# Performance work log

Measured on AMD Instinct MI355X. Metric: run time of the kernel, lower is better.

The kernel has to match this reference:

```python
import jax, jax.numpy as jnp
import numpy as np

B, N, D = 8, 4096, 1024
DEPTH, HEADS, DH = 4, 16, 64
INNER = HEADS * DH          # 1024
NL, NMP = 64, 4             # latents, mean-pooled latents
FF = 4 * D                  # ff_mult=4
EPS = 1e-5


def _ln(x, w, b):
    # nn.LayerNorm over last dim (eps added to biased variance)
    m = x.mean(-1, keepdims=True)
    v = ((x - m) ** 2).mean(-1, keepdims=True)
    return (x - m) * jax.lax.rsqrt(v + EPS) * w + b


def _ln_g(x, g):
    # custom LayerNorm: gamma only, no bias
    m = x.mean(-1, keepdims=True)
    v = ((x - m) ** 2).mean(-1, keepdims=True)
    return (x - m) * jax.lax.rsqrt(v + EPS) * g


def setup_inputs() -> dict:
    key = jax.random.key(0)
    ks = jax.random.split(key, 16)
    g = lambda i, shape: jax.random.normal(ks[i], shape, jnp.float32) * 0.02
    return dict(
        x=jax.random.normal(ks[0], (B, N, D), jnp.float32),
        pos_emb=g(1, (N, D)),                      # rows [0:N] of the embedding table
        latents=jax.random.normal(ks[2], (NL, D), jnp.float32),
        mp_ln_g=jnp.ones((D,), jnp.float32),
        mp_w=g(3, (D, D * NMP)),
        mp_b=jnp.zeros((D * NMP,), jnp.float32),
        ln_x_w=jnp.ones((DEPTH, D), jnp.float32),
        ln_x_b=jnp.zeros((DEPTH, D), jnp.float32),
        ln_lat_w=jnp.ones((DEPTH, D), jnp.float32),
        ln_lat_b=jnp.zeros((DEPTH, D), jnp.float32),
        wq=g(4, (DEPTH, D, INNER)),
        wkv=g(5, (DEPTH, D, 2 * INNER)),
        wo=g(6, (DEPTH, INNER, D)),
        out_ln_w=jnp.ones((DEPTH, D), jnp.float32),
        out_ln_b=jnp.zeros((DEPTH, D), jnp.float32),
        ff_ln1_g=jnp.ones((DEPTH, D), jnp.float32),
        ff_w1=g(7, (DEPTH, D, FF)),
        ff_ln2_g=jnp.ones((DEPTH, FF), jnp.float32),
        ff_w2=g(8, (DEPTH, FF, D)),
    )


def reference(x, pos_emb, latents, mp_ln_g, mp_w, mp_b,
              ln_x_w, ln_x_b, ln_lat_w, ln_lat_b, wq, wkv, wo,
              out_ln_w, out_ln_b, ff_ln1_g, ff_w1, ff_ln2_g, ff_w2):
    b = x.shape[0]
    xp = x + pos_emb                                  # (b, n, d)
    lat = jnp.broadcast_to(latents, (b,) + latents.shape)
    # mean-pooled latents (mask is all-ones -> plain mean over tokens)
    mp = x.mean(axis=1)                               # (b, d)
    mp_lat = (_ln_g(mp, mp_ln_g) @ mp_w + mp_b).reshape(b, NMP, D)
    lat = jnp.concatenate([mp_lat, lat], axis=1)      # (b, NMP+NL, d)
    scale = DH ** -0.5
    for l in range(DEPTH):
        # --- PerceiverAttention ---
        xn = _ln(xp, ln_x_w[l], ln_x_b[l])
        ln_lat = _ln(lat, ln_lat_w[l], ln_lat_b[l])
        q = (ln_lat @ wq[l]).reshape(b, -1, HEADS, DH) * scale   # (b, i, h, dh)
        kv = jnp.concatenate([xn, ln_lat], axis=1) @ wkv[l]      # (b, n+i, 2*inner)
        k, v = jnp.split(kv, 2, axis=-1)
        k = k.reshape(b, -1, HEADS, DH)
        v = v.reshape(b, -1, HEADS, DH)
        sim = jnp.einsum('bihd,bjhd->bhij', q, k)                # (b, h, i, n+i)
        attn = jax.nn.softmax(sim, axis=-1)
        o = jnp.einsum('bhij,bjhd->bihd', attn, v).reshape(b, -1, INNER)
        o = _ln(o @ wo[l], out_ln_w[l], out_ln_b[l])
        lat = lat + o
        # --- feedforward block ---
        h = jax.nn.gelu(_ln_g(lat, ff_ln1_g[l]) @ ff_w1[l], approximate=False)
        lat = lat + _ln_g(h, ff_ln2_g[l]) @ ff_w2[l]
    return lat
```

## Files before the change

kernel.cpp:

```cpp
#include <hip/hip_runtime.h>

typedef __bf16 bf16x8 __attribute__((ext_vector_type(8)));
typedef float f32x4 __attribute__((ext_vector_type(4)));
typedef unsigned short u16;
typedef unsigned int u32;

typedef __attribute__((address_space(3))) u16 lds_u16;
typedef __attribute__((address_space(1))) const u16 glb_u16;

#define NJC 4

__device__ inline float bf2f(u16 u) { union { u32 i; float f; } x; x.i = (u32)u << 16; return x.f; }
__device__ inline u16 f2bf(float f) {
  union { float f; u32 i; } u; u.f = f;
  u32 r = u.i + 0x7fffu + ((u.i >> 16) & 1u);
  return (u16)(r >> 16);
}

__device__ inline float blk_sum256(float v, float* red) {
#pragma unroll
  for (int o = 32; o > 0; o >>= 1) v += __shfl_xor(v, o);
  __syncthreads();
  if ((threadIdx.x & 63) == 0) red[threadIdx.x >> 6] = v;
  __syncthreads();
  return red[0] + red[1] + red[2] + red[3];
}

__global__ __launch_bounds__(512, 1) void gemm_kv(const u16* __restrict__ A,
                                                  const u16* __restrict__ BT,
                                                  u16* __restrict__ C,
                                                  const float* __restrict__ bias) {
  extern __shared__ __align__(16) u16 lds[];
  const int tid = threadIdx.x, l = tid & 63, w = tid >> 6;
  const int wr = w >> 2, wc = w & 3;
  int bid = blockIdx.x;
  int swz = (bid & 7) * 128 + (bid >> 3);
  int by = swz >> 3, bx = swz & 7;
  const long m0 = (long)by * 256;
  const int n0 = bx * 256;

  long srcA[2], srcB[2];
#pragma unroll
  for (int s = 0; s < 2; s++) {
    int g = s * 512 + tid;
    int p = g >> 3, j = g & 7, jp = j ^ (p & 7);
    int row = (p << 1) | (jp >> 2), cc = jp & 3;
    srcA[s] = (m0 + row) * 1024 + cc * 8;
    srcB[s] = ((long)(n0 + row)) * 1024 + cc * 8;
  }
  const int ldsoff[2] = { (w * 64) * 8, (512 + w * 64) * 8 };

  const int rA = l & 15, cch = l >> 4;
  const int R0a = wr * 128 + rA;
  const int aoff = (R0a >> 1) * 64 + (((((R0a & 1) << 2) | cch) ^ ((R0a >> 1) & 7)) << 3);
  const int R0b = wc * 64 + rA;
  const int boff = (R0b >> 1) * 64 + (((((R0b & 1) << 2) | cch) ^ ((R0b >> 1) & 7)) << 3);

  f32x4 acc[8][4] = {};

  auto stage = [&](int t, int ab) {
    u16* dst = lds + (((t & 3) * 2 + ab) << 13);
    const u16* src = ab == 0 ? A : BT;
    const long* so = ab == 0 ? srcA : srcB;
    int kt = t * 32;
#pragma unroll
    for (int s = 0; s < 2; s++)
      __builtin_amdgcn_global_load_lds((glb_u16*)(src + so[s] + kt),
                                       (lds_u16*)(dst + ldsoff[s]), 16, 0, 0);
  };

  stage(0, 0); stage(0, 1); stage(1, 0); stage(1, 1); stage(2, 0); stage(2, 1);
  asm volatile("s_waitcnt vmcnt(8)" ::: "memory");
  __builtin_amdgcn_s_barrier();

  for (int t = 0; t < 16; ++t) {
    const int s = 2 * t;
    const u16* Ab0 = lds + (((s & 3) * 2 + 0) << 13);
    const u16* Bb0 = lds + (((s & 3) * 2 + 1) << 13);
    const u16* Ab1 = lds + ((((s + 1) & 3) * 2 + 0) << 13);
    const u16* Bb1 = lds + ((((s + 1) & 3) * 2 + 1) << 13);
    bf16x8 af[8], b0, b1;

#pragma unroll
    for (int mf = 0; mf < 8; mf++) af[mf] = *(const bf16x8*)(Ab0 + aoff + mf * 512);
    b0 = *(const bf16x8*)(Bb0 + boff);
    b1 = *(const bf16x8*)(Bb0 + boff + 512);
    if (s + 3 < 32) stage(s + 3, 0);
    __builtin_amdgcn_s_barrier();
    asm volatile("s_waitcnt lgkmcnt(0)" ::: "memory");
    __builtin_amdgcn_sched_barrier(0);
    __builtin_amdgcn_s_setprio(1);
#pragma unroll
    for (int mf = 0; mf < 8; mf++) {
      acc[mf][0] = __builtin_amdgcn_mfma_f32_16x16x32_bf16(af[mf], b0, acc[mf][0], 0, 0, 0);
      acc[mf][1] = __builtin_amdgcn_mfma_f32_16x16x32_bf16(af[mf], b1, acc[mf][1], 0, 0, 0);
    }
    __builtin_amdgcn_s_setprio(0);
    __builtin_amdgcn_s_barrier();

    b0 = *(const bf16x8*)(Bb0 + boff + 1024);
    b1 = *(const bf16x8*)(Bb0 + boff + 1536);
    if (s + 3 < 32) stage(s + 3, 1);
    __builtin_amdgcn_s_barrier();
    asm volatile("s_waitcnt lgkmcnt(0)" ::: "memory");
    __builtin_amdgcn_sched_barrier(0);
    __builtin_amdgcn_s_setprio(1);
#pragma unroll
    for (int mf = 0; mf < 8; mf++) {
      acc[mf][2] = __builtin_amdgcn_mfma_f32_16x16x32_bf16(af[mf], b0, acc[mf][2], 0, 0, 0);
      acc[mf][3] = __builtin_amdgcn_mfma_f32_16x16x32_bf16(af[mf], b1, acc[mf][3], 0, 0, 0);
    }
    __builtin_amdgcn_s_setprio(0);
    if (t < 15) asm volatile("s_waitcnt vmcnt(8)" ::: "memory");
    else        asm volatile("s_waitcnt vmcnt(0)" ::: "memory");
    __builtin_amdgcn_s_barrier();

#pragma unroll
    for (int mf = 0; mf < 8; mf++) af[mf] = *(const bf16x8*)(Ab1 + aoff + mf * 512);
    b0 = *(const bf16x8*)(Bb1 + boff);
    b1 = *(const bf16x8*)(Bb1 + boff + 512);
    if (s + 4 < 32) stage(s + 4, 0);
    __builtin_amdgcn_s_barrier();
    asm volatile("s_waitcnt lgkmcnt(0)" ::: "memory");
    __builtin_amdgcn_sched_barrier(0);
    __builtin_amdgcn_s_setprio(1);
#pragma unroll
    for (int mf = 0; mf < 8; mf++) {
      acc[mf][0] = __builtin_amdgcn_mfma_f32_16x16x32_bf16(af[mf], b0, acc[mf][0], 0, 0, 0);
      acc[mf][1] = __builtin_amdgcn_mfma_f32_16x16x32_bf16(af[mf], b1, acc[mf][1], 0, 0, 0);
    }
    __builtin_amdgcn_s_setprio(0);
    __builtin_amdgcn_s_barrier();

    b0 = *(const bf16x8*)(Bb1 + boff + 1024);
    b1 = *(const bf16x8*)(Bb1 + boff + 1536);
    if (s + 4 < 32) stage(s + 4, 1);
    __builtin_amdgcn_s_barrier();
    asm volatile("s_waitcnt lgkmcnt(0)" ::: "memory");
    __builtin_amdgcn_sched_barrier(0);
    __builtin_amdgcn_s_setprio(1);
#pragma unroll
    for (int mf = 0; mf < 8; mf++) {
      acc[mf][2] = __builtin_amdgcn_mfma_f32_16x16x32_bf16(af[mf], b0, acc[mf][2], 0, 0, 0);
      acc[mf][3] = __builtin_amdgcn_mfma_f32_16x16x32_bf16(af[mf], b1, acc[mf][3], 0, 0, 0);
    }
    __builtin_amdgcn_s_setprio(0);
    if (t < 14)       asm volatile("s_waitcnt vmcnt(8)" ::: "memory");
    else if (t == 14) asm volatile("s_waitcnt vmcnt(4)" ::: "memory");
    __builtin_amdgcn_s_barrier();
  }

  const long batch_off = (m0 >> 12) * ((long)4164 * 2048);
  const int rb0 = (int)(m0 & 4095) + wr * 128 + ((l >> 4) << 2);
#pragma unroll
  for (int mf = 0; mf < 8; mf++) {
#pragma unroll
    for (int nf = 0; nf < 4; nf++) {
      int col = n0 + wc * 64 + nf * 16 + (l & 15);
      float bv = bias[col];
#pragma unroll
      for (int rr = 0; rr < 4; rr++) {
        int rloc = rb0 + mf * 16 + rr;
        C[batch_off + (long)rloc * 2048 + col] = f2bf(acc[mf][nf][rr] + bv);
      }
    }
  }
}

template <int MODE, bool BIAS>
__global__ __launch_bounds__(256) void gemm_nt(const u16* __restrict__ A,
                                               const u16* __restrict__ BT,
                                               void* __restrict__ C,
                                               const float* __restrict__ bias,
                                               int M, int N, int K, float alpha,
                                               int RB, long BS, int LDC, int KC) {
  __shared__ __align__(16) u16 As[128 * 64];
  __shared__ __align__(16) u16 Bs[128 * 64];
  int m0 = blockIdx.y * 128, n0 = blockIdx.x * 128;
  int tid = threadIdx.x;
  int l = tid & 63, w = tid >> 6;
  int wr = w >> 1, wc = w & 1;
  f32x4 acc[4][4] = {};

  const int srow = l >> 3;
  const int scol = (l & 7) * 8;
  const int Mc = M - 1;
  const int k0 = blockIdx.z * KC;
  const int k1 = (k0 + KC < K) ? k0 + KC : K;

  for (int kt = k0; kt < k1; kt += 64) {
#pragma unroll
    for (int r = 0; r < 4; r++) {
      int rowg = (r * 4 + w) * 8;
      int arow = m0 + rowg + srow; if (arow > Mc) arow = Mc;
      int brow = n0 + rowg + srow;
      const u16* ag = A + (long)arow * K + kt + scol;
      const u16* bg = BT + (long)brow * K + kt + scol;
      __builtin_amdgcn_global_load_lds((glb_u16*)ag, (lds_u16*)(As + rowg * 64), 16, 0, 0);
      __builtin_amdgcn_global_load_lds((glb_u16*)bg, (lds_u16*)(Bs + rowg * 64), 16, 0, 0);
    }
    __syncthreads();
#pragma unroll
    for (int kk = 0; kk < 2; kk++) {
      bf16x8 af[4], bfv[4];
#pragma unroll
      for (int mf = 0; mf < 4; mf++)
        af[mf] = *(const bf16x8*)(As + (wr * 64 + mf * 16 + (l & 15)) * 64 + kk * 32 + (l >> 4) * 8);
#pragma unroll
      for (int nf = 0; nf < 4; nf++)
        bfv[nf] = *(const bf16x8*)(Bs + (wc * 64 + nf * 16 + (l & 15)) * 64 + kk * 32 + (l >> 4) * 8);
#pragma unroll
      for (int mf = 0; mf < 4; mf++)
#pragma unroll
        for (int nf = 0; nf < 4; nf++)
          acc[mf][nf] = __builtin_amdgcn_mfma_f32_16x16x32_bf16(af[mf], bfv[nf], acc[mf][nf], 0, 0, 0);
    }
    __syncthreads();
  }

#pragma unroll
  for (int mf = 0; mf < 4; mf++) {
#pragma unroll
    for (int nf = 0; nf < 4; nf++) {
      int col = n0 + wc * 64 + nf * 16 + (l & 15);
      float bv = 0.f;
      if (BIAS) bv = bias[col];
#pragma unroll
      for (int rr = 0; rr < 4; rr++) {
        int row = m0 + wr * 64 + mf * 16 + (l >> 4) * 4 + rr;
        if (row < M) {
          float v = acc[mf][nf][rr] * alpha + bv;
          long off = (long)(row / RB) * BS + (long)(row % RB) * LDC + col;
          if (MODE == 0) ((float*)C)[off] = v;
          else if (MODE == 1) ((u16*)C)[off] = f2bf(v);
          else if (MODE == 2) ((float*)C)[off] += v;
          else atomicAdd(&((float*)C)[off], v);
        }
      }
    }
  }
}

__global__ __launch_bounds__(256) void gemm_two(const u16* __restrict__ A,
                                                const u16* __restrict__ BTq,
                                                const u16* __restrict__ BTkv,
                                                u16* __restrict__ Cq,
                                                u16* __restrict__ Ckv) {
  __shared__ __align__(16) u16 As[128 * 64];
  __shared__ __align__(16) u16 Bs[128 * 64];
  const int K = 1024, M = 544;
  int bxr = blockIdx.x;
  const u16* BT; u16* C; float alpha; int RB; long BS; int LDC; int n0;
  if (bxr < 8) { BT = BTq;  C = Cq;  alpha = 0.125f; RB = 544; BS = 0;                 LDC = 1024; n0 = bxr * 128; }
  else         { BT = BTkv; C = Ckv; alpha = 1.f;    RB = 68;  BS = (long)4164 * 2048; LDC = 2048; n0 = (bxr - 8) * 128; }
  int m0 = blockIdx.y * 128;
  int tid = threadIdx.x;
  int l = tid & 63, w = tid >> 6;
  int wr = w >> 1, wc = w & 1;
  f32x4 acc[4][4] = {};

  const int srow = l >> 3;
  const int scol = (l & 7) * 8;
  const int Mc = M - 1;

  for (int kt = 0; kt < K; kt += 64) {
#pragma unroll
    for (int r = 0; r < 4; r++) {
      int rowg = (r * 4 + w) * 8;
      int arow = m0 + rowg + srow; if (arow > Mc) arow = Mc;
      int brow = n0 + rowg + srow;
      const u16* ag = A + (long)arow * K + kt + scol;
      const u16* bg = BT + (long)brow * K + kt + scol;
      __builtin_amdgcn_global_load_lds((glb_u16*)ag, (lds_u16*)(As + rowg * 64), 16, 0, 0);
      __builtin_amdgcn_global_load_lds((glb_u16*)bg, (lds_u16*)(Bs + rowg * 64), 16, 0, 0);
    }
    __syncthreads();
#pragma unroll
    for (int kk = 0; kk < 2; kk++) {
      bf16x8 af[4], bfv[4];
#pragma unroll
      for (int mf = 0; mf < 4; mf++)
        af[mf] = *(const bf16x8*)(As + (wr * 64 + mf * 16 + (l & 15)) * 64 + kk * 32 + (l >> 4) * 8);
#pragma unroll
      for (int nf = 0; nf < 4; nf++)
        bfv[nf] = *(const bf16x8*)(Bs + (wc * 64 + nf * 16 + (l & 15)) * 64 + kk * 32 + (l >> 4) * 8);
#pragma unroll
      for (int mf = 0; mf < 4; mf++)
#pragma unroll
        for (int nf = 0; nf < 4; nf++)
          acc[mf][nf] = __builtin_amdgcn_mfma_f32_16x16x32_bf16(af[mf], bfv[nf], acc[mf][nf], 0, 0, 0);
    }
    __syncthreads();
  }

#pragma unroll
  for (int mf = 0; mf < 4; mf++) {
#pragma unroll
    for (int nf = 0; nf < 4; nf++) {
      int col = n0 + wc * 64 + nf * 16 + (l & 15);
#pragma unroll
      for (int rr = 0; rr < 4; rr++) {
        int row = m0 + wr * 64 + mf * 16 + (l >> 4) * 4 + rr;
        if (row < M) {
          float v = acc[mf][nf][rr] * alpha;
          long off = (long)(row / RB) * BS + (long)(row % RB) * LDC + col;
          C[off] = f2bf(v);
        }
      }
    }
  }
}

__global__ __launch_bounds__(256) void k_transpose(const float* __restrict__ W,
                                                   const float* __restrict__ scale,
                                                   u16* __restrict__ WT, int K, int N,
                                                   long wls, long sls, long tls) {
  __shared__ float tile[32][33];
  int z = blockIdx.z;
  W += (long)z * wls; WT += (long)z * tls;
  if (scale) scale += (long)z * sls;
  int n0 = blockIdx.x * 32, k0 = blockIdx.y * 32;
  int x = threadIdx.x, y = threadIdx.y;
#pragma unroll
  for (int i = 0; i < 4; i++) tile[y + 8 * i][x] = W[(long)(k0 + y + 8 * i) * N + n0 + x];
  __syncthreads();
#pragma unroll
  for (int i = 0; i < 4; i++) {
    int k = k0 + x, n = n0 + y + 8 * i;
    float v = tile[x][y + 8 * i];
    if (scale) v *= scale[k];
    WT[(long)n * K + k] = f2bf(v);
  }
}

__global__ __launch_bounds__(256) void k_transpose2(const float* __restrict__ W,
                                                    const float* __restrict__ scale,
                                                    u16* __restrict__ WTs,
                                                    u16* __restrict__ WTp, int K, int N,
                                                    long wls, long sls, long tls) {
  __shared__ float tile[32][33];
  int z = blockIdx.z;
  W += (long)z * wls; scale += (long)z * sls;
  WTs += (long)z * tls; WTp += (long)z * tls;
  int n0 = blockIdx.x * 32, k0 = blockIdx.y * 32;
  int x = threadIdx.x, y = threadIdx.y;
#pragma unroll
  for (int i = 0; i < 4; i++) tile[y + 8 * i][x] = W[(long)(k0 + y + 8 * i) * N + n0 + x];
  __syncthreads();
#pragma unroll
  for (int i = 0; i < 4; i++) {
    int k = k0 + x, n = n0 + y + 8 * i;
    float v = tile[x][y + 8 * i];
    WTp[(long)n * K + k] = f2bf(v);
    WTs[(long)n * K + k] = f2bf(v * scale[k]);
  }
}

__global__ __launch_bounds__(256) void k_xphat(const float* __restrict__ x,
                                               const float* __restrict__ pos,
                                               u16* __restrict__ xph) {
  __shared__ float red[4];
  long row = blockIdx.x;
  int n = blockIdx.x & 4095;
  const float* xr = x + row * 1024;
  const float* pr = pos + (long)n * 1024;
  float v[4]; float s = 0.f;
#pragma unroll
  for (int i = 0; i < 4; i++) { int c = threadIdx.x + i * 256; v[i] = xr[c] + pr[c]; s += v[i]; }
  float mean = blk_sum256(s, red) * (1.f / 1024.f);
  float s2 = 0.f;
#pragma unroll
  for (int i = 0; i < 4; i++) { float d = v[i] - mean; s2 += d * d; }
  float rs = rsqrtf(blk_sum256(s2, red) * (1.f / 1024.f) + 1e-5f);
#pragma unroll
  for (int i = 0; i < 4; i++) xph[row * 1024 + threadIdx.x + i * 256] = f2bf((v[i] - mean) * rs);
}

__global__ __launch_bounds__(256) void k_mp(const float* __restrict__ x, float* __restrict__ macc) {
  int d = blockIdx.x * 256 + threadIdx.x;
  int nc = blockIdx.y, b = blockIdx.z;
  const float* xb = x + (long)b * 4096 * 1024;
  float s = 0.f;
  for (int n = nc * 256; n < nc * 256 + 256; n++) s += xb[(long)n * 1024 + d];
  atomicAdd(&macc[b * 1024 + d], s);
}

__global__ __launch_bounds__(256) void k_mphat(const float* __restrict__ macc,
                                               const float* __restrict__ g,
                                               float* __restrict__ mphat) {
  __shared__ float red[4];
  int b = blockIdx.x;
  float v[4]; float s = 0.f;
#pragma unroll
  for (int i = 0; i < 4; i++) { v[i] = macc[b * 1024 + threadIdx.x + i * 256] * (1.f / 4096.f); s += v[i]; }
  float mean = blk_sum256(s, red) * (1.f / 1024.f);
  float s2 = 0.f;
#pragma unroll
  for (int i = 0; i < 4; i++) { float d = v[i] - mean; s2 += d * d; }
  float rs = rsqrtf(blk_sum256(s2, red) * (1.f / 1024.f) + 1e-5f);
#pragma unroll
  for (int i = 0; i < 4; i++) {
    int c = threadIdx.x + i * 256;
    mphat[b * 1024 + c] = (v[i] - mean) * rs * g[c];
  }
}

__global__ __launch_bounds__(256) void k_mplat(const float* __restrict__ mphat,
                                               const float* __restrict__ w,
                                               const float* __restrict__ bias,
                                               float* __restrict__ lat) {
  int j = blockIdx.x * 256 + threadIdx.x;
  int b = blockIdx.y;
  const float* mh = mphat + b * 1024;
  float s = bias[j];
  for (int k = 0; k < 1024; k++) s += mh[k] * w[(long)k * 4096 + j];
  lat[(long)b * 69632 + (j >> 10) * 1024 + (j & 1023)] = s;
}

__global__ __launch_bounds__(256) void k_latfill(const float* __restrict__ latents,
                                                 float* __restrict__ lat) {
  int idx = blockIdx.x * 256 + threadIdx.x;
  int b = idx >> 16, rest = idx & 65535;
  lat[(long)b * 69632 + 4096 + rest] = latents[rest];
}

__global__ __launch_bounds__(256) void k_lnrow(const float* __restrict__ in,
                                               const float* __restrict__ w,
                                               const float* __restrict__ bb,
                                               u16* __restrict__ out) {
  __shared__ float red[4];
  long row = blockIdx.x;
  const float* xr = in + row * 1024;
  float v[4]; float s = 0.f;
#pragma unroll
  for (int i = 0; i < 4; i++) { v[i] = xr[threadIdx.x + i * 256]; s += v[i]; }
  float mean = blk_sum256(s, red) * (1.f / 1024.f);
  float s2 = 0.f;
#pragma unroll
  for (int i = 0; i < 4; i++) { float d = v[i] - mean; s2 += d * d; }
  float rs = rsqrtf(blk_sum256(s2, red) * (1.f / 1024.f) + 1e-5f);
#pragma unroll
  for (int i = 0; i < 4; i++) {
    int c = threadIdx.x + i * 256;
    out[row * 1024 + c] = f2bf((v[i] - mean) * rs * w[c] + bb[c]);
  }
}

__global__ __launch_bounds__(256) void k_bias1(const float* __restrict__ wkv,
                                               const float* __restrict__ lnxb,
                                               float* __restrict__ bxp,
                                               long wls, long bls, long pls) {
  int z = blockIdx.z;
  wkv += (long)z * wls; lnxb += (long)z * bls; bxp += (long)z * pls;
  int n = blockIdx.x * 256 + threadIdx.x;
  int kc = blockIdx.y;
  float s = 0.f;
  for (int k = kc * 64; k < kc * 64 + 64; k++) s += lnxb[k] * wkv[(long)k * 2048 + n];
  bxp[kc * 2048 + n] = s;
}
__global__ __launch_bounds__(256) void k_bias2(const float* __restrict__ bxp,
                                               float* __restrict__ bx,
                                               long pls, long xls) {
  int z = blockIdx.y;
  bxp += (long)z * pls; bx += (long)z * xls;
  int n = blockIdx.x * 256 + threadIdx.x;
  float s = 0.f;
#pragma unroll
  for (int kc = 0; kc < 16; kc++) s += bxp[kc * 2048 + n];
  bx[n] = s;
}

__global__ __launch_bounds__(256) void k_flash(const u16* __restrict__ q,
                                               const u16* __restrict__ kv,
                                               float* __restrict__ opart,
                                               float* __restrict__ lpart) {
  int c = blockIdx.x, h = blockIdx.y, b = blockIdx.z;
  int tid = threadIdx.x, l = tid & 63, w = tid >> 6;

  __shared__ __align__(16) char smem_raw[46080];
  u16 (*Vt)[64][40] = reinterpret_cast<u16(*)[64][40]>(smem_raw);
  u16 (*Pl)[80][40] = reinterpret_cast<u16(*)[80][40]>(smem_raw + 20480);
  float (*O_s)[64] = reinterpret_cast<float(*)[64]>(smem_raw);
  float* l_s = reinterpret_cast<float*>(smem_raw + 20480);

  const int JCH = 1041;
  const int jstart = c * JCH;
  const int jend = (c == NJC - 1) ? 4164 : jstart + JCH;
  const long kvbase = (long)b * 4164 * 2048;
  const u16* Kp = kv + kvbase + h * 64;
  const u16* Vp = kv + kvbase + 1024 + h * 64;

  bf16x8 qf[5][2];
#pragma unroll
  for (int it = 0; it < 5; it++) {
    int qi = it * 16 + (l & 15); if (qi > 67) qi = 67;
    const u16* qrow = q + ((long)(b * 68 + qi) * 1024 + h * 64 + (l >> 4) * 8);
    qf[it][0] = *(const bf16x8*)(qrow);
    qf[it][1] = *(const bf16x8*)(qrow + 32);
  }

  f32x4 Of[5][4] = {};
  float lac[5] = {0.f, 0.f, 0.f, 0.f, 0.f};

  auto loadV = [&](int j0, uint4 vv[4]) {
#pragma unroll
    for (int t = 0; t < 4; t++) {
      int vj = j0 + (l & 31);
      int vjc = vj < 4163 ? vj : 4163;
      int vd = (l >> 5) * 8 + t * 16;
      vv[t] = *(const uint4*)(Vp + (long)vjc * 2048 + vd);
    }
  };
  auto loadK = [&](int j0, bf16x8& a00, bf16x8& a01, bf16x8& a10, bf16x8& a11) {
    const u16* kr0 = Kp + (long)(j0 + (l & 15)) * 2048 + (l >> 4) * 8;
    a00 = *(const bf16x8*)(kr0);
    a01 = *(const bf16x8*)(kr0 + 32);
    const u16* kr1 = Kp + (long)(j0 + 16 + (l & 15)) * 2048 + (l >> 4) * 8;
    a10 = *(const bf16x8*)(kr1);
    a11 = *(const bf16x8*)(kr1 + 32);
  };

  const int jbeg = jstart + w * 32;
  uint4 vr[4];
  bf16x8 k0a, k0b, k1a, k1b;
  if (jbeg < jend) { loadV(jbeg, vr); loadK(jbeg, k0a, k0b, k1a, k1b); }

  for (int j0 = jbeg; j0 < jend; j0 += 4 * 32) {
#pragma unroll
    for (int t = 0; t < 4; t++) {
      int vd = (l >> 5) * 8 + t * 16;
      union { uint4 q4; u16 s[8]; } uu; uu.q4 = vr[t];
#pragma unroll
      for (int e = 0; e < 8; e++) Vt[w][vd + e][l & 31] = uu.s[e];
    }
    f32x4 sf[2][5];
#pragma unroll
    for (int it = 0; it < 5; it++) {
      f32x4 d0 = {};
      d0 = __builtin_amdgcn_mfma_f32_16x16x32_bf16(k0a, qf[it][0], d0, 0, 0, 0);
      d0 = __builtin_amdgcn_mfma_f32_16x16x32_bf16(k0b, qf[it][1], d0, 0, 0, 0);
      sf[0][it] = d0;
      f32x4 d1 = {};
      d1 = __builtin_amdgcn_mfma_f32_16x16x32_bf16(k1a, qf[it][0], d1, 0, 0, 0);
      d1 = __builtin_amdgcn_mfma_f32_16x16x32_bf16(k1b, qf[it][1], d1, 0, 0, 0);
      sf[1][it] = d1;
    }
    int jn = j0 + 4 * 32;
    bool more = jn < jend;
    uint4 vr2[4];
    bf16x8 n0a, n0b, n1a, n1b;
    if (more) { loadV(jn, vr2); loadK(jn, n0a, n0b, n1a, n1b); }
#pragma unroll
    for (int jt = 0; jt < 2; jt++) {
      int jb = j0 + jt * 16 + (l >> 4) * 4;
#pragma unroll
      for (int it = 0; it < 5; it++) {
        u16 pk[4];
#pragma unroll
        for (int r = 0; r < 4; r++) {
          float p = (jb + r < jend) ? __expf(sf[jt][it][r]) : 0.f;
          lac[it] += p;
          pk[r] = f2bf(p);
        }
        *(uint2*)(&Pl[w][it * 16 + (l & 15)][jt * 16 + (l >> 4) * 4]) = *(const uint2*)pk;
      }
    }
#pragma unroll
    for (int it = 0; it < 5; it++) {
      bf16x8 pa = *(const bf16x8*)(&Pl[w][it * 16 + (l & 15)][(l >> 4) * 8]);
#pragma unroll
      for (int dt = 0; dt < 4; dt++) {
        bf16x8 vb = *(const bf16x8*)(&Vt[w][dt * 16 + (l & 15)][(l >> 4) * 8]);
        Of[it][dt] = __builtin_amdgcn_mfma_f32_16x16x32_bf16(pa, vb, Of[it][dt], 0, 0, 0);
      }
    }
    if (more) {
      vr[0] = vr2[0]; vr[1] = vr2[1]; vr[2] = vr2[2]; vr[3] = vr2[3];
      k0a = n0a; k0b = n0b; k1a = n1a; k1b = n1b;
    }
  }

  __syncthreads();
  for (int u = tid; u < 80 * 64; u += 256) ((float*)O_s)[u] = 0.f;
  if (tid < 80) l_s[tid] = 0.f;
  __syncthreads();
#pragma unroll
  for (int it = 0; it < 5; it++) {
    float v = lac[it];
    v += __shfl_xor(v, 16);
    v += __shfl_xor(v, 32);
    if (l < 16) atomicAdd(&l_s[it * 16 + l], v);
#pragma unroll
    for (int dt = 0; dt < 4; dt++) {
#pragma unroll
      for (int r = 0; r < 4; r++) {
        int i = it * 16 + (l >> 4) * 4 + r;
        int d = dt * 16 + (l & 15);
        atomicAdd(&O_s[i][d], Of[it][dt][r]);
      }
    }
  }
  __syncthreads();
  long base = (long)((b * 16 + h) * NJC + c);
  for (int u = tid; u < 68 * 64; u += 256)
    opart[base * 68 * 64 + u] = O_s[u >> 6][u & 63];
  if (tid < 68) lpart[base * 68 + tid] = l_s[tid];
}

__global__ __launch_bounds__(256) void k_comb(const float* __restrict__ opart,
                                              const float* __restrict__ lpart,
                                              u16* __restrict__ obf,
                                              float* __restrict__ o2z) {
  int r = blockIdx.x;
  int b = r / 68, i = r % 68;
#pragma unroll
  for (int it = 0; it < 4; it++) {
    int col = threadIdx.x + it * 256;
    int h = col >> 6, d = col & 63;
    long bh = (long)(b * 16 + h) * NJC;
    float os = 0.f, ls = 0.f;
    for (int cc = 0; cc < NJC; cc++) {
      os += opart[(bh + cc) * 68 * 64 + (long)i * 64 + d];
      ls += lpart[(bh + cc) * 68 + i];
    }
    obf[(long)r * 1024 + col] = f2bf(os / ls);
    o2z[(long)r * 1024 + col] = 0.f;
  }
}

__global__ __launch_bounds__(256) void k_attnln(const float* __restrict__ o2,
                                                float* __restrict__ lat,
                                                const float* __restrict__ w,
                                                const float* __restrict__ bb,
                                                const float* __restrict__ g,
                                                u16* __restrict__ latg) {
  __shared__ float red[4];
  long row = blockIdx.x;
  const float* xr = o2 + row * 1024;
  float* lr = lat + row * 1024;
  float v[4]; float s = 0.f;
#pragma unroll
  for (int i = 0; i < 4; i++) { v[i] = xr[threadIdx.x + i * 256]; s += v[i]; }
  float mean = blk_sum256(s, red) * (1.f / 1024.f);
  float s2 = 0.f;
#pragma unroll
  for (int i = 0; i < 4; i++) { float d = v[i] - mean; s2 += d * d; }
  float rs = rsqrtf(blk_sum256(s2, red) * (1.f / 1024.f) + 1e-5f);
  float lv[4]; float sl = 0.f;
#pragma unroll
  for (int i = 0; i < 4; i++) {
    int c = threadIdx.x + i * 256;
    float t = (v[i] - mean) * rs * w[c] + bb[c];
    lv[i] = lr[c] + t;
    lr[c] = lv[i];
    sl += lv[i];
  }
  float mean2 = blk_sum256(sl, red) * (1.f / 1024.f);
  float s22 = 0.f;
#pragma unroll
  for (int i = 0; i < 4; i++) { float d = lv[i] - mean2; s22 += d * d; }
  float rs2 = rsqrtf(blk_sum256(s22, red) * (1.f / 1024.f) + 1e-5f);
#pragma unroll
  for (int i = 0; i < 4; i++) {
    int c = threadIdx.x + i * 256;
    latg[row * 1024 + c] = f2bf((lv[i] - mean2) * rs2 * g[c]);
  }
}

__global__ __launch_bounds__(256) void k_geluln(const float* __restrict__ hin,
                                                const float* __restrict__ g,
                                                u16* __restrict__ out) {
  __shared__ float red[4];
  long row = blockIdx.x;
  const float* xr = hin + row * 4096;
  float v[16]; float s = 0.f;
#pragma unroll
  for (int i = 0; i < 16; i++) {
    int c = threadIdx.x + i * 256;
    float u = xr[c];
    u = 0.5f * u * (1.f + erff(u * 0.70710678118f));
    v[i] = u; s += u;
  }
  float mean = blk_sum256(s, red) * (1.f / 4096.f);
  float s2 = 0.f;
#pragma unroll
  for (int i = 0; i < 16; i++) { float d = v[i] - mean; s2 += d * d; }
  float rs = rsqrtf(blk_sum256(s2, red) * (1.f / 4096.f) + 1e-5f);
#pragma unroll
  for (int i = 0; i < 16; i++) {
    int c = threadIdx.x + i * 256;
    out[row * 4096 + c] = f2bf((v[i] - mean) * rs * g[c]);
  }
}

extern "C" void kernel_launch(void* const* d_in, const int* in_sizes, int n_in,
                              void* d_out, int out_size, void* d_ws, size_t ws_size,
                              hipStream_t stream) {
  const float* x    = (const float*)d_in[0];
  const float* pos  = (const float*)d_in[1];
  const float* lats = (const float*)d_in[2];
  const float* mplng= (const float*)d_in[3];
  const float* mpw  = (const float*)d_in[4];
  const float* mpb  = (const float*)d_in[5];
  const float* lnxw = (const float*)d_in[6];
  const float* lnxb = (const float*)d_in[7];
  const float* lnlw = (const float*)d_in[8];
  const float* lnlb = (const float*)d_in[9];
  const float* wq   = (const float*)d_in[10];
  const float* wkv  = (const float*)d_in[11];
  const float* wo   = (const float*)d_in[12];
  const float* olnw = (const float*)d_in[13];
  const float* olnb = (const float*)d_in[14];
  const float* ffg1 = (const float*)d_in[15];
  const float* ffw1 = (const float*)d_in[16];
  const float* ffg2 = (const float*)d_in[17];
  const float* ffw2 = (const float*)d_in[18];

  char* ws = (char*)d_ws;
  size_t off = 0;
  auto take = [&](size_t n) -> char* {
    off = (off + 255) & ~(size_t)255;
    char* p = ws + off; off += n; return p;
  };
  float* mp_acc = (float*)take(8 * 1024 * 4);
  float* mp_hat = (float*)take(8 * 1024 * 4);
  u16*   xp_hat = (u16*)take((size_t)8 * 4096 * 1024 * 2);
  float* lat    = (float*)take((size_t)8 * 68 * 1024 * 4);
  u16*   lnlat  = (u16*)take((size_t)544 * 1024 * 2);
  u16*   qb     = (u16*)take((size_t)544 * 1024 * 2);
  u16*   kvb    = (u16*)take(((size_t)8 * 4164 + 64) * 2048 * 2);
  float* opart  = (float*)take((size_t)128 * NJC * 68 * 64 * 4);
  float* lpart  = (float*)take((size_t)128 * NJC * 68 * 4);
  u16*   obf    = (u16*)take((size_t)544 * 1024 * 2);
  float* o2     = (float*)take((size_t)544 * 1024 * 4);
  u16*   latg   = (u16*)take((size_t)544 * 1024 * 2);
  float* hbuf   = (float*)take((size_t)544 * 4096 * 4);
  u16*   hg     = (u16*)take((size_t)544 * 4096 * 2);

  size_t fixed_off = off;
  u16 *wqT, *wkvxT, *wkvlT, *woT, *ffw1T, *ffw2T;
  float *bx, *bxp;
  auto alloc_w = [&](size_t rep) {
    wqT   = (u16*)take(rep * (size_t)1024 * 1024 * 2);
    wkvxT = (u16*)take(rep * (size_t)2048 * 1024 * 2);
    wkvlT = (u16*)take(rep * (size_t)2048 * 1024 * 2);
    woT   = (u16*)take(rep * (size_t)1024 * 1024 * 2);
    ffw1T = (u16*)take(rep * (size_t)4096 * 1024 * 2);
    ffw2T = (u16*)take(rep * (size_t)4096 * 1024 * 2);
    bx    = (float*)take(rep * 2048 * 4);
    bxp   = (float*)take(rep * 16 * 2048 * 4);
  };
  alloc_w(4);
  bool hoist = off <= ws_size;
  if (!hoist) { off = fixed_off; alloc_w(1); }

  const long KV_BS = (long)4164 * 2048;

  hipMemsetAsync(mp_acc, 0, 8 * 1024 * 4, stream);
  k_xphat<<<32768, 256, 0, stream>>>(x, pos, xp_hat);
  k_mp<<<dim3(4, 16, 8), 256, 0, stream>>>(x, mp_acc);
  k_mphat<<<8, 256, 0, stream>>>(mp_acc, mplng, mp_hat);
  k_mplat<<<dim3(16, 8), 256, 0, stream>>>(mp_hat, mpw, mpb, lat);
  k_latfill<<<2048, 256, 0, stream>>>(lats, lat);

  if (hoist) {
    k_transpose<<<dim3(32, 32, 4), dim3(32, 8), 0, stream>>>(
        wq, nullptr, wqT, 1024, 1024, 1048576, 0, 1048576);
    k_transpose2<<<dim3(64, 32, 4), dim3(32, 8), 0, stream>>>(
        wkv, lnxw, wkvxT, wkvlT, 1024, 2048, 2097152, 1024, 2097152);
    k_transpose<<<dim3(32, 32, 4), dim3(32, 8), 0, stream>>>(
        wo, nullptr, woT, 1024, 1024, 1048576, 0, 1048576);
    k_transpose<<<dim3(128, 32, 4), dim3(32, 8), 0, stream>>>(
        ffw1, nullptr, ffw1T, 1024, 4096, 4194304, 0, 4194304);
    k_transpose<<<dim3(32, 128, 4), dim3(32, 8), 0, stream>>>(
        ffw2, nullptr, ffw2T, 4096, 1024, 4194304, 0, 4194304);
    k_bias1<<<dim3(8, 16, 4), 256, 0, stream>>>(wkv, lnxb, bxp, 2097152, 1024, 32768);
    k_bias2<<<dim3(8, 4), 256, 0, stream>>>(bxp, bx, 32768, 2048);
  }

  for (int l = 0; l < 4; l++) {
    const float* wq_l  = wq  + (size_t)l * 1024 * 1024;
    const float* wkv_l = wkv + (size_t)l * 1024 * 2048;
    const float* wo_l  = wo  + (size_t)l * 1024 * 1024;
    const float* w1_l  = ffw1 + (size_t)l * 1024 * 4096;
    const float* w2_l  = ffw2 + (size_t)l * 4096 * 1024;

    if (!hoist) {
      k_transpose<<<dim3(32, 32, 1), dim3(32, 8), 0, stream>>>(
          wq_l, nullptr, wqT, 1024, 1024, 0, 0, 0);
      k_transpose2<<<dim3(64, 32, 1), dim3(32, 8), 0, stream>>>(
          wkv_l, lnxw + l * 1024, wkvxT, wkvlT, 1024, 2048, 0, 0, 0);
      k_transpose<<<dim3(32, 32, 1), dim3(32, 8), 0, stream>>>(
          wo_l, nullptr, woT, 1024, 1024, 0, 0, 0);
      k_transpose<<<dim3(128, 32, 1), dim3(32, 8), 0, stream>>>(
          w1_l, nullptr, ffw1T, 1024, 4096, 0, 0, 0);
      k_transpose<<<dim3(32, 128, 1), dim3(32, 8), 0, stream>>>(
          w2_l, nullptr, ffw2T, 4096, 1024, 0, 0, 0);
      k_bias1<<<dim3(8, 16, 1), 256, 0, stream>>>(wkv_l, lnxb + l * 1024, bxp, 0, 0, 0);
      k_bias2<<<dim3(8, 1), 256, 0, stream>>>(bxp, bx, 0, 0);
    }
    const u16* wqT_l   = wqT   + (hoist ? (size_t)l * 1048576 : 0);
    const u16* wkvxT_l = wkvxT + (hoist ? (size_t)l * 2097152 : 0);
    const u16* wkvlT_l = wkvlT + (hoist ? (size_t)l * 2097152 : 0);
    const u16* woT_l   = woT   + (hoist ? (size_t)l * 1048576 : 0);
    const u16* ffw1T_l = ffw1T + (hoist ? (size_t)l * 4194304 : 0);
    const u16* ffw2T_l = ffw2T + (hoist ? (size_t)l * 4194304 : 0);
    const float* bx_l  = bx    + (hoist ? (size_t)l * 2048 : 0);

    k_lnrow<<<544, 256, 0, stream>>>(lat, lnlw + l * 1024, lnlb + l * 1024, lnlat);

    gemm_kv<<<1024, 512, 131072, stream>>>(xp_hat, wkvxT_l, kvb, bx_l);
    gemm_two<<<dim3(24, 5), 256, 0, stream>>>(lnlat, wqT_l, wkvlT_l, qb, kvb + (size_t)4096 * 2048);

    k_flash<<<dim3(NJC, 16, 8), 256, 0, stream>>>(qb, kvb, opart, lpart);
    k_comb<<<544, 256, 0, stream>>>(opart, lpart, obf, o2);

    gemm_nt<3, false><<<dim3(8, 5, 4), 256, 0, stream>>>(
        obf, woT_l, o2, nullptr, 544, 1024, 1024, 1.f, 544, 0, 1024, 256);
    k_attnln<<<544, 256, 0, stream>>>(o2, lat, olnw + l * 1024, olnb + l * 1024,
                                      ffg1 + l * 1024, latg);
    gemm_nt<0, false><<<dim3(32, 5, 1), 256, 0, stream>>>(
        latg, ffw1T_l, hbuf, nullptr, 544, 4096, 1024, 1.f, 544, 0, 4096, 1024);
    k_geluln<<<544, 256, 0, stream>>>(hbuf, ffg2 + l * 4096, hg);
    gemm_nt<3, false><<<dim3(8, 5, 8), 256, 0, stream>>>(
        hg, ffw2T_l, lat, nullptr, 544, 1024, 4096, 1.f, 544, 0, 1024, 512);
  }

  hipMemcpyAsync(d_out, lat, (size_t)out_size * 4, hipMemcpyDeviceToDevice, stream);
}
```

Before: 1.623 ms.

## Double-buffer LDS tiles in gemm_nt and gemm_two to overlap loads with MFMA

Gives the GEMM kernels two LDS buffers per operand and issues the global-to-LDS loads for the next K tile before computing the current one. Explicit vmcnt waits and s_barrier replace __syncthreads, so the loads of the following stage can overlap the MFMA work. LDS use per block doubles to 64 KB, which may reduce occupancy. Correctness depends on the vmcnt(8) count matching the eight loads issued per stage.

```diff
diff --git a/kernel.cpp b/kernel.cpp
--- a/kernel.cpp
+++ b/kernel.cpp
@@ -174,8 +174,8 @@
                                                const float* __restrict__ bias,
                                                int M, int N, int K, float alpha,
                                                int RB, long BS, int LDC, int KC) {
-  __shared__ __align__(16) u16 As[128 * 64];
-  __shared__ __align__(16) u16 Bs[128 * 64];
+  __shared__ __align__(16) u16 As[2][128 * 64];
+  __shared__ __align__(16) u16 Bs[2][128 * 64];
   int m0 = blockIdx.y * 128, n0 = blockIdx.x * 128;
   int tid = threadIdx.x;
   int l = tid & 63, w = tid >> 6;
@@ -188,7 +188,7 @@
   const int k0 = blockIdx.z * KC;
   const int k1 = (k0 + KC < K) ? k0 + KC : K;
 
-  for (int kt = k0; kt < k1; kt += 64) {
+  auto stage = [&](int kt, int pb) {
 #pragma unroll
     for (int r = 0; r < 4; r++) {
       int rowg = (r * 4 + w) * 8;
@@ -196,26 +196,40 @@
       int brow = n0 + rowg + srow;
       const u16* ag = A + (long)arow * K + kt + scol;
       const u16* bg = BT + (long)brow * K + kt + scol;
-      __builtin_amdgcn_global_load_lds((glb_u16*)ag, (lds_u16*)(As + rowg * 64), 16, 0, 0);
-      __builtin_amdgcn_global_load_lds((glb_u16*)bg, (lds_u16*)(Bs + rowg * 64), 16, 0, 0);
-    }
-    __syncthreads();
+      __builtin_amdgcn_global_load_lds((glb_u16*)ag, (lds_u16*)(&As[pb][rowg * 64]), 16, 0, 0);
+      __builtin_amdgcn_global_load_lds((glb_u16*)bg, (lds_u16*)(&Bs[pb][rowg * 64]), 16, 0, 0);
+    }
+  };
+
+  stage(k0, 0);
+  int it = 0;
+  for (int kt = k0; kt < k1; kt += 64, ++it) {
+    const int pb = it & 1;
+    const bool more = (kt + 64) < k1;
+    if (more) stage(kt + 64, pb ^ 1);
+    if (more) asm volatile("s_waitcnt vmcnt(8)" ::: "memory");
+    else      asm volatile("s_waitcnt vmcnt(0)" ::: "memory");
+    __builtin_amdgcn_sched_barrier(0);
+    __builtin_amdgcn_s_barrier();
+    const u16* Ab = &As[pb][0];
+    const u16* Bb = &Bs[pb][0];
 #pragma unroll
     for (int kk = 0; kk < 2; kk++) {
       bf16x8 af[4], bfv[4];
 #pragma unroll
       for (int mf = 0; mf < 4; mf++)
-        af[mf] = *(const bf16x8*)(As + (wr * 64 + mf * 16 + (l & 15)) * 64 + kk * 32 + (l >> 4) * 8);
+        af[mf] = *(const bf16x8*)(Ab + (wr * 64 + mf * 16 + (l & 15)) * 64 + kk * 32 + (l >> 4) * 8);
 #pragma unroll
       for (int nf = 0; nf < 4; nf++)
-        bfv[nf] = *(const bf16x8*)(Bs + (wc * 64 + nf * 16 + (l & 15)) * 64 + kk * 32 + (l >> 4) * 8);
+        bfv[nf] = *(const bf16x8*)(Bb + (wc * 64 + nf * 16 + (l & 15)) * 64 + kk * 32 + (l >> 4) * 8);
 #pragma unroll
       for (int mf = 0; mf < 4; mf++)
 #pragma unroll
         for (int nf = 0; nf < 4; nf++)
           acc[mf][nf] = __builtin_amdgcn_mfma_f32_16x16x32_bf16(af[mf], bfv[nf], acc[mf][nf], 0, 0, 0);
     }
-    __syncthreads();
+    __builtin_amdgcn_sched_barrier(0);
+    __builtin_amdgcn_s_barrier();
   }
 
 #pragma unroll
@@ -246,8 +260,8 @@
                                                 const u16* __restrict__ BTkv,
                                                 u16* __restrict__ Cq,
                                                 u16* __restrict__ Ckv) {
-  __shared__ __align__(16) u16 As[128 * 64];
-  __shared__ __align__(16) u16 Bs[128 * 64];
+  __shared__ __align__(16) u16 As[2][128 * 64];
+  __shared__ __align__(16) u16 Bs[2][128 * 64];
   const int K = 1024, M = 544;
   int bxr = blockIdx.x;
   const u16* BT; u16* C; float alpha; int RB; long BS; int LDC; int n0;
@@ -263,7 +277,7 @@
   const int scol = (l & 7) * 8;
   const int Mc = M - 1;
 
-  for (int kt = 0; kt < K; kt += 64) {
+  auto stage = [&](int kt, int pb) {
 #pragma unroll
     for (int r = 0; r < 4; r++) {
       int rowg = (r * 4 + w) * 8;
@@ -271,26 +285,40 @@
       int brow = n0 + rowg + srow;
       const u16* ag = A + (long)arow * K + kt + scol;
       const u16* bg = BT + (long)brow * K + kt + scol;
-      __builtin_amdgcn_global_load_lds((glb_u16*)ag, (lds_u16*)(As + rowg * 64), 16, 0, 0);
-      __builtin_amdgcn_global_load_lds((glb_u16*)bg, (lds_u16*)(Bs + rowg * 64), 16, 0, 0);
-    }
-    __syncthreads();
+      __builtin_amdgcn_global_load_lds((glb_u16*)ag, (lds_u16*)(&As[pb][rowg * 64]), 16, 0, 0);
+      __builtin_amdgcn_global_load_lds((glb_u16*)bg, (lds_u16*)(&Bs[pb][rowg * 64]), 16, 0, 0);
+    }
+  };
+
+  stage(0, 0);
+  int it = 0;
+  for (int kt = 0; kt < K; kt += 64, ++it) {
+    const int pb = it & 1;
+    const bool more = (kt + 64) < K;
+    if (more) stage(kt + 64, pb ^ 1);
+    if (more) asm volatile("s_waitcnt vmcnt(8)" ::: "memory");
+    else      asm volatile("s_waitcnt vmcnt(0)" ::: "memory");
+    __builtin_amdgcn_sched_barrier(0);
+    __builtin_amdgcn_s_barrier();
+    const u16* Ab = &As[pb][0];
+    const u16* Bb = &Bs[pb][0];
 #pragma unroll
     for (int kk = 0; kk < 2; kk++) {
       bf16x8 af[4], bfv[4];
 #pragma unroll
       for (int mf = 0; mf < 4; mf++)
-        af[mf] = *(const bf16x8*)(As + (wr * 64 + mf * 16 + (l & 15)) * 64 + kk * 32 + (l >> 4) * 8);
+        af[mf] = *(const bf16x8*)(Ab + (wr * 64 + mf * 16 + (l & 15)) * 64 + kk * 32 + (l >> 4) * 8);
 #pragma unroll
       for (int nf = 0; nf < 4; nf++)
-        bfv[nf] = *(const bf16x8*)(Bs + (wc * 64 + nf * 16 + (l & 15)) * 64 + kk * 32 + (l >> 4) * 8);
+        bfv[nf] = *(const bf16x8*)(Bb + (wc * 64 + nf * 16 + (l & 15)) * 64 + kk * 32 + (l >> 4) * 8);
 #pragma unroll
       for (int mf = 0; mf < 4; mf++)
 #pragma unroll
         for (int nf = 0; nf < 4; nf++)
           acc[mf][nf] = __builtin_amdgcn_mfma_f32_16x16x32_bf16(af[mf], bfv[nf], acc[mf][nf], 0, 0, 0);
     }
-    __syncthreads();
+    __builtin_amdgcn_sched_barrier(0);
+    __builtin_amdgcn_s_barrier();
   }
 
 #pragma unroll
```

New measurement: 1.611 ms. Within noise of the previous version (-0.7%).
